# Optimization experiments

Measured on AMD Instinct MI355X. Metric: run time of the kernel, lower is better.

Reference implementation:

```python
import jax, jax.numpy as jnp
import numpy as np

B, S, E, H = 8, 1024, 1024, 16
D = E // H  # head_dim = hidden_size // num_heads


def setup_inputs() -> dict:
    key = jax.random.key(0)
    ks = jax.random.split(key, 9)
    s = 0.02
    return {
        "h":  jax.random.normal(ks[0], (B, S, E), jnp.float32),
        # per-head projection weights stacked over heads; torch Linear(E, D) -> stored [E, D] (x @ W)
        "Wq": jax.random.normal(ks[1], (H, E, D), jnp.float32) * s,
        "bq": jax.random.normal(ks[2], (H, D), jnp.float32) * s,
        "Wk": jax.random.normal(ks[3], (H, E, D), jnp.float32) * s,
        "bk": jax.random.normal(ks[4], (H, D), jnp.float32) * s,
        "Wv": jax.random.normal(ks[5], (H, E, D), jnp.float32) * s,  # dead weight: original passes h as value
        "bv": jax.random.normal(ks[6], (H, D), jnp.float32) * s,
        "Wo": jax.random.normal(ks[7], (E, E), jnp.float32) * s,
        "bo": jax.random.normal(ks[8], (E,), jnp.float32) * s,
    }


def reference(h, Wq, bq, Wk, bk, Wv, bv, Wo, bo):
    # Batched over all heads at once instead of the original Python loop.
    q = jnp.einsum('bse,hed->bhsd', h, Wq) + bq[None, :, None, :]   # [B,H,S,D]
    k = jnp.einsum('bse,hed->bhsd', h, Wk) + bk[None, :, None, :]   # [B,H,S,D]
    # v is computed in the original module but NOT used (do_attention gets h as value)
    _v = jnp.einsum('bse,hed->bhsd', h, Wv) + bv[None, :, None, :]
    scale = 1.0 / jnp.sqrt(jnp.asarray(D, h.dtype))
    scores = jnp.einsum('bhsd,bhtd->bhst', q, k) * scale            # [B,H,S,T]
    # original: F.softmax(scores, dim=1) on per-head [B,S,T] -> query axis = axis 2 here
    weights = jax.nn.softmax(scores, axis=2)
    ctx = jnp.einsum('bhst,bte->bhse', weights, h)                  # value = h (embed_dim), per original
    # torch.cat over dim=1 of per-head [B,S,E] outputs -> [B, H*S, E]
    x = ctx.reshape(B, H * S, E)
    return x @ Wo + bo
```

## Files before the change

kernel.cpp:

```cpp
#include <hip/hip_runtime.h>

#define B_ 8
#define S_ 1024
#define E_ 1024
#define H_ 16
#define D_ 64

typedef __attribute__((ext_vector_type(8))) __bf16 bf16x8;
typedef __attribute__((ext_vector_type(4))) float f32x4;
typedef __attribute__((ext_vector_type(4))) unsigned short u16x4;
typedef __attribute__((ext_vector_type(8))) unsigned short u16x8;

static __device__ __forceinline__ unsigned short f2bf(float f) {
  union { float f; unsigned int u; } v; v.f = f;
  unsigned int r = v.u + 0x7FFFu + ((v.u >> 16) & 1u);
  return (unsigned short)(r >> 16);
}

#define MFMA16(a, b, c) __builtin_amdgcn_mfma_f32_16x16x32_bf16((a), (b), (c), 0, 0, 0)

__global__ void cast_f32_bf16_kernel(const float* __restrict__ src,
                                     unsigned short* __restrict__ dst, int n4) {
  int i = blockIdx.x * 256 + threadIdx.x;
  if (i >= n4) return;
  float4 v = reinterpret_cast<const float4*>(src)[i];
  u16x4 o;
  o[0] = f2bf(v.x); o[1] = f2bf(v.y); o[2] = f2bf(v.z); o[3] = f2bf(v.w);
  reinterpret_cast<u16x4*>(dst)[i] = o;
}

__global__ void transpose_cast_kernel(const float* __restrict__ src,
                                      unsigned short* __restrict__ dst,
                                      int rows, int cols) {
  __shared__ unsigned short tile[64][65];
  const float* s = src + (size_t)blockIdx.z * rows * cols;
  unsigned short* d = dst + (size_t)blockIdx.z * rows * cols;
  int rb = blockIdx.y * 64, cb = blockIdx.x * 64;
#pragma unroll
  for (int k = 0; k < 16; k++) {
    int idx = threadIdx.x + 256 * k;
    int r = idx >> 6, c = idx & 63;
    tile[r][c] = f2bf(s[(size_t)(rb + r) * cols + cb + c]);
  }
  __syncthreads();
#pragma unroll
  for (int k = 0; k < 16; k++) {
    int idx = threadIdx.x + 256 * k;
    int r = idx >> 6, c = idx & 63;
    d[(size_t)(cb + r) * rows + rb + c] = tile[c][r];
  }
}

__launch_bounds__(256)
__global__ void gemm_G_kernel(const unsigned short* __restrict__ hb,
                              const unsigned short* __restrict__ WoT,
                              unsigned short* __restrict__ Gt) {
  int mblk = blockIdx.x, nblk = blockIdx.y, b = blockIdx.z;
  const unsigned short* A = hb + (size_t)b * S_ * E_;
  int tid = threadIdx.x, l = tid & 63, w = tid >> 6;
  int ws = w & 1, wc = w >> 1, lr = l & 15, lg = l >> 4;
  f32x4 acc[4][4] = {};
  int ar[4], bc[4];
#pragma unroll
  for (int i = 0; i < 4; i++) ar[i] = mblk * 128 + ws * 64 + i * 16 + lr;
#pragma unroll
  for (int j = 0; j < 4; j++) bc[j] = nblk * 128 + wc * 64 + j * 16 + lr;
  for (int k0 = 0; k0 < E_; k0 += 32) {
    bf16x8 a[4], bb[4];
#pragma unroll
    for (int i = 0; i < 4; i++)
      a[i] = *reinterpret_cast<const bf16x8*>(A + (size_t)ar[i] * E_ + k0 + lg * 8);
#pragma unroll
    for (int j = 0; j < 4; j++)
      bb[j] = *reinterpret_cast<const bf16x8*>(WoT + (size_t)bc[j] * E_ + k0 + lg * 8);
#pragma unroll
    for (int i = 0; i < 4; i++)
#pragma unroll
      for (int j = 0; j < 4; j++)
        acc[i][j] = MFMA16(a[i], bb[j], acc[i][j]);
  }
#pragma unroll
  for (int i = 0; i < 4; i++) {
    int t0 = mblk * 128 + ws * 64 + i * 16 + lg * 4;
#pragma unroll
    for (int j = 0; j < 4; j++) {
      u16x4 p;
#pragma unroll
      for (int r = 0; r < 4; r++) p[r] = f2bf(acc[i][j][r]);
      int e = bc[j];
      size_t addr = (((size_t)b * 4 + (e >> 8)) * 32 + (t0 >> 5)) * 8192 +
                    (size_t)(e & 255) * 32 + (t0 & 31);
      *reinterpret_cast<u16x4*>(Gt + addr) = p;
    }
  }
}

__launch_bounds__(256)
__global__ void proj_qk_kernel(const unsigned short* __restrict__ hb,
                               const unsigned short* __restrict__ WqT,
                               const unsigned short* __restrict__ WkT,
                               const float* __restrict__ bq,
                               const float* __restrict__ bk,
                               unsigned short* __restrict__ Qb,
                               unsigned short* __restrict__ Kb) {
  int sblk = blockIdx.x, z = blockIdx.y;
  int b = z >> 4, h = z & 15;
  const unsigned short* A = hb + (size_t)b * S_ * E_;
  const unsigned short* Btq = WqT + (size_t)h * D_ * E_;
  const unsigned short* Btk = WkT + (size_t)h * D_ * E_;
  int tid = threadIdx.x, l = tid & 63, w = tid >> 6;
  int ws = w & 1, wc = w >> 1, lr = l & 15, lg = l >> 4;
  f32x4 accq[4][2] = {}, acck[4][2] = {};
  int ar[4], bc[2];
#pragma unroll
  for (int i = 0; i < 4; i++) ar[i] = sblk * 128 + ws * 64 + i * 16 + lr;
#pragma unroll
  for (int j = 0; j < 2; j++) bc[j] = wc * 32 + j * 16 + lr;
  for (int k0 = 0; k0 < E_; k0 += 32) {
    bf16x8 a[4], bbq[2], bbk[2];
#pragma unroll
    for (int i = 0; i < 4; i++)
      a[i] = *reinterpret_cast<const bf16x8*>(A + (size_t)ar[i] * E_ + k0 + lg * 8);
#pragma unroll
    for (int j = 0; j < 2; j++) {
      bbq[j] = *reinterpret_cast<const bf16x8*>(Btq + (size_t)bc[j] * E_ + k0 + lg * 8);
      bbk[j] = *reinterpret_cast<const bf16x8*>(Btk + (size_t)bc[j] * E_ + k0 + lg * 8);
    }
#pragma unroll
    for (int i = 0; i < 4; i++)
#pragma unroll
      for (int j = 0; j < 2; j++) {
        accq[i][j] = MFMA16(a[i], bbq[j], accq[i][j]);
        acck[i][j] = MFMA16(a[i], bbk[j], acck[i][j]);
      }
  }
  unsigned short* oq = Qb + (size_t)z * S_ * D_;
  unsigned short* ok = Kb + (size_t)z * S_ * D_;
#pragma unroll
  for (int j = 0; j < 2; j++) {
    float bvq = bq[h * D_ + bc[j]], bvk = bk[h * D_ + bc[j]];
#pragma unroll
    for (int i = 0; i < 4; i++)
#pragma unroll
      for (int r = 0; r < 4; r++) {
        int s = sblk * 128 + ws * 64 + i * 16 + lg * 4 + r;
        oq[(size_t)s * D_ + bc[j]] = f2bf(accq[i][j][r] + bvq);
        ok[(size_t)s * D_ + bc[j]] = f2bf(acck[i][j][r] + bvk);
      }
  }
}

__launch_bounds__(256)
__global__ void stats_kernel(const unsigned short* __restrict__ Qb,
                             const unsigned short* __restrict__ Kb,
                             float* __restrict__ c) {
  int tblk = blockIdx.x, z = blockIdx.y;
  const unsigned short* Q = Qb + (size_t)z * S_ * D_;
  const unsigned short* K = Kb + (size_t)z * S_ * D_;
  int tid = threadIdx.x, l = tid & 63, w = tid >> 6;
  int lr = l & 15, lg = l >> 4;
  int tb = tblk * 256 + w * 64;
  const float scale = 0.125f;
  bf16x8 kb[4][2];
#pragma unroll
  for (int j = 0; j < 4; j++)
#pragma unroll
    for (int ks = 0; ks < 2; ks++)
      kb[j][ks] = *reinterpret_cast<const bf16x8*>(
          K + (size_t)(tb + j * 16 + lr) * D_ + ks * 32 + lg * 8);
  float m[4], zz[4];
#pragma unroll
  for (int j = 0; j < 4; j++) { m[j] = -1e30f; zz[j] = 0.f; }
  for (int s0 = 0; s0 < S_; s0 += 32) {
    bf16x8 aq[2][2];
#pragma unroll
    for (int sf = 0; sf < 2; sf++)
#pragma unroll
      for (int ks = 0; ks < 2; ks++)
        aq[sf][ks] = *reinterpret_cast<const bf16x8*>(
            Q + (size_t)(s0 + sf * 16 + lr) * D_ + ks * 32 + lg * 8);
    f32x4 acc[2][4] = {};
#pragma unroll
    for (int sf = 0; sf < 2; sf++)
#pragma unroll
      for (int j = 0; j < 4; j++) {
        acc[sf][j] = MFMA16(aq[sf][0], kb[j][0], acc[sf][j]);
        acc[sf][j] = MFMA16(aq[sf][1], kb[j][1], acc[sf][j]);
      }
#pragma unroll
    for (int j = 0; j < 4; j++) {
      float v[8];
#pragma unroll
      for (int sf = 0; sf < 2; sf++)
#pragma unroll
        for (int r = 0; r < 4; r++) v[sf * 4 + r] = acc[sf][j][r] * scale;
      float mx = m[j];
#pragma unroll
      for (int t = 0; t < 8; t++) mx = fmaxf(mx, v[t]);
      float sum = 0.f;
#pragma unroll
      for (int t = 0; t < 8; t++) sum += __expf(v[t] - mx);
      zz[j] = zz[j] * __expf(m[j] - mx) + sum;
      m[j] = mx;
    }
  }
#pragma unroll
  for (int j = 0; j < 4; j++) {
    float mj = m[j], zj = zz[j];
#pragma unroll
    for (int off = 16; off <= 32; off <<= 1) {
      float om = __shfl_xor(mj, off, 64);
      float oz = __shfl_xor(zj, off, 64);
      float mn = fmaxf(mj, om);
      zj = zj * __expf(mj - mn) + oz * __expf(om - mn);
      mj = mn;
    }
    if (l < 16) c[(size_t)z * S_ + tb + j * 16 + lr] = mj + __logf(zj);
  }
}

__launch_bounds__(256, 2)
__global__ void attn_kernel(const unsigned short* __restrict__ Qb,
                            const unsigned short* __restrict__ Kb,
                            const unsigned short* __restrict__ Gt,
                            const float* __restrict__ cst,
                            const float* __restrict__ bo,
                            float* __restrict__ out) {
  int sblk = blockIdx.x, eblk = blockIdx.y, z = blockIdx.z;
  int b = z >> 4, h = z & 15;
  __shared__ unsigned short Ks[2][32][72];
  __shared__ unsigned short Gs[256][40];
  __shared__ unsigned short Ps[128][40];
  int tid = threadIdx.x, l = tid & 63, w = tid >> 6;
  int lr = l & 15, lg = l >> 4;
  int ws = w & 1, we = w >> 1;
  const unsigned short* Q = Qb + (size_t)z * S_ * D_ + (size_t)sblk * 128 * D_;
  const unsigned short* K = Kb + (size_t)z * S_ * D_;
  const unsigned short* Gb = Gt + (((size_t)b * 4 + eblk) * 32) * 8192;
  const float* cz = cst + (size_t)z * S_;
  const float scale = 0.125f;

  bf16x8 q[2][2];
#pragma unroll
  for (int sf = 0; sf < 2; sf++)
#pragma unroll
    for (int ks = 0; ks < 2; ks++)
      q[sf][ks] = *reinterpret_cast<const bf16x8*>(
          Q + (size_t)(w * 32 + sf * 16 + lr) * D_ + ks * 32 + lg * 8);

  int krow = tid >> 3, kc8 = (tid & 7) * 8;
  u16x8 kreg, greg[4];

  kreg = *reinterpret_cast<const u16x8*>(K + (size_t)krow * D_ + kc8);
#pragma unroll
  for (int i = 0; i < 4; i++)
    greg[i] = *reinterpret_cast<const u16x8*>(Gb + (tid + 256 * i) * 8);
  *reinterpret_cast<u16x8*>(&Ks[0][krow][kc8]) = kreg;
#pragma unroll
  for (int i = 0; i < 4; i++) {
    int cid = tid + 256 * i;
    *reinterpret_cast<u16x8*>(&Gs[cid >> 2][(cid & 3) * 8]) = greg[i];
  }
  kreg = *reinterpret_cast<const u16x8*>(K + (size_t)(32 + krow) * D_ + kc8);
#pragma unroll
  for (int i = 0; i < 4; i++)
    greg[i] = *reinterpret_cast<const u16x8*>(Gb + 8192 + (tid + 256 * i) * 8);
  __syncthreads();

  f32x4 acc[4][8] = {};

  for (int it = 0; it < 32; ++it) {
    int cur = it & 1, nxt = cur ^ 1;
    int t0 = it * 32;
    *reinterpret_cast<u16x8*>(&Ks[nxt][krow][kc8]) = kreg;
    {
      int tk = t0 + 64; if (tk >= S_) tk = 0;
      kreg = *reinterpret_cast<const u16x8*>(K + (size_t)(tk + krow) * D_ + kc8);
    }
    {
      bf16x8 ka[2][2];
#pragma unroll
      for (int tf = 0; tf < 2; tf++)
#pragma unroll
        for (int ks = 0; ks < 2; ks++)
          ka[tf][ks] = *reinterpret_cast<const bf16x8*>(&Ks[cur][tf * 16 + lr][ks * 32 + lg * 8]);
      f32x4 sa[2][2] = {};
#pragma unroll
      for (int tf = 0; tf < 2; tf++)
#pragma unroll
        for (int sf = 0; sf < 2; sf++) {
          sa[tf][sf] = MFMA16(ka[tf][0], q[sf][0], sa[tf][sf]);
          sa[tf][sf] = MFMA16(ka[tf][1], q[sf][1], sa[tf][sf]);
        }
#pragma unroll
      for (int tf = 0; tf < 2; tf++) {
        f32x4 cv = *reinterpret_cast<const f32x4*>(cz + t0 + tf * 16 + lg * 4);
#pragma unroll
        for (int sf = 0; sf < 2; sf++) {
          u16x4 p;
#pragma unroll
          for (int r = 0; r < 4; r++)
            p[r] = f2bf(__expf(sa[tf][sf][r] * scale - cv[r]));
          *reinterpret_cast<u16x4*>(&Ps[w * 32 + sf * 16 + lr][tf * 16 + lg * 4]) = p;
        }
      }
    }
    __syncthreads();
    {
      bf16x8 ap[4], bg[8];
#pragma unroll
      for (int i = 0; i < 4; i++)
        ap[i] = *reinterpret_cast<const bf16x8*>(&Ps[ws * 64 + i * 16 + lr][lg * 8]);
#pragma unroll
      for (int j = 0; j < 8; j++)
        bg[j] = *reinterpret_cast<const bf16x8*>(&Gs[we * 128 + j * 16 + lr][lg * 8]);
      __builtin_amdgcn_s_setprio(1);
#pragma unroll
      for (int i = 0; i < 4; i++)
#pragma unroll
        for (int j = 0; j < 8; j++)
          acc[i][j] = MFMA16(ap[i], bg[j], acc[i][j]);
      __builtin_amdgcn_s_setprio(0);
    }
    __syncthreads();
    {
#pragma unroll
      for (int i = 0; i < 4; i++) {
        int cid = tid + 256 * i;
        *reinterpret_cast<u16x8*>(&Gs[cid >> 2][(cid & 3) * 8]) = greg[i];
      }
      int tg = (it + 2) & 31;
#pragma unroll
      for (int i = 0; i < 4; i++)
        greg[i] = *reinterpret_cast<const u16x8*>(Gb + (size_t)tg * 8192 + (tid + 256 * i) * 8);
    }
  }

  float bov[8];
#pragma unroll
  for (int j = 0; j < 8; j++) bov[j] = bo[eblk * 256 + we * 128 + j * 16 + lr];
#pragma unroll
  for (int i = 0; i < 4; i++)
#pragma unroll
    for (int j = 0; j < 8; j++)
#pragma unroll
      for (int r = 0; r < 4; r++) {
        int srow = sblk * 128 + ws * 64 + i * 16 + lg * 4 + r;
        size_t R = (size_t)h * S_ + srow;
        int col = eblk * 256 + we * 128 + j * 16 + lr;
        out[((size_t)b * (H_ * S_) + R) * E_ + col] = acc[i][j][r] + bov[j];
      }
}

extern "C" void kernel_launch(void* const* d_in, const int* in_sizes, int n_in,
                              void* d_out, int out_size, void* d_ws, size_t ws_size,
                              hipStream_t stream) {
  const float* h  = (const float*)d_in[0];
  const float* Wq = (const float*)d_in[1];
  const float* bq = (const float*)d_in[2];
  const float* Wk = (const float*)d_in[3];
  const float* bk = (const float*)d_in[4];
  const float* Wo = (const float*)d_in[7];
  const float* bo = (const float*)d_in[8];
  float* out = (float*)d_out;

  char* p = (char*)d_ws;
  unsigned short* hb  = (unsigned short*)p; p += (size_t)B_ * S_ * E_ * 2;
  unsigned short* WoT = (unsigned short*)p; p += (size_t)E_ * E_ * 2;
  unsigned short* WqT = (unsigned short*)p; p += (size_t)H_ * D_ * E_ * 2;
  unsigned short* WkT = (unsigned short*)p; p += (size_t)H_ * D_ * E_ * 2;
  unsigned short* Qb  = (unsigned short*)p; p += (size_t)B_ * H_ * S_ * D_ * 2;
  unsigned short* Kb  = (unsigned short*)p; p += (size_t)B_ * H_ * S_ * D_ * 2;
  unsigned short* Gt  = (unsigned short*)p; p += (size_t)B_ * E_ * S_ * 2;
  float*          cst = (float*)p;          p += (size_t)B_ * H_ * S_ * 4;

  int n4 = B_ * S_ * E_ / 4;
  cast_f32_bf16_kernel<<<dim3(n4 / 256), 256, 0, stream>>>(h, hb, n4);
  transpose_cast_kernel<<<dim3(16, 16, 1), 256, 0, stream>>>(Wo, WoT, E_, E_);
  transpose_cast_kernel<<<dim3(1, 16, H_), 256, 0, stream>>>(Wq, WqT, E_, D_);
  transpose_cast_kernel<<<dim3(1, 16, H_), 256, 0, stream>>>(Wk, WkT, E_, D_);
  gemm_G_kernel<<<dim3(8, 8, B_), 256, 0, stream>>>(hb, WoT, Gt);
  proj_qk_kernel<<<dim3(8, B_ * H_), 256, 0, stream>>>(hb, WqT, WkT, bq, bk, Qb, Kb);
  stats_kernel<<<dim3(S_ / 256, B_ * H_), 256, 0, stream>>>(Qb, Kb, cst);
  attn_kernel<<<dim3(8, 4, B_ * H_), 256, 0, stream>>>(Qb, Kb, Gt, cst, bo, out);
}
```

Measured before the change: 691.2 us.

## Software-pipeline attention loop with double-buffered P/G and direct K loads

Restructures the attention kernel main loop so the P·G MFMA for window it-1 runs alongside the QK^T score and exp computation for window it. P and G are double-buffered in shared memory, which cuts the barriers per iteration from two to one, and the K tile is read straight from global memory into registers instead of being staged through LDS. It also swaps the software bf16 rounding for a hardware conversion and uses exp2 with a pre-scaled log-sum-exp constant. The cost is more LDS use, which may lower occupancy, plus possibly higher global-load latency for K.

Measured after the change: 745.7 us. +7.9%, slower.

```diff
diff --git a/kernel.cpp b/kernel.cpp
--- a/kernel.cpp
+++ b/kernel.cpp
@@ -11,11 +11,18 @@
 typedef __attribute__((ext_vector_type(4))) unsigned short u16x4;
 typedef __attribute__((ext_vector_type(8))) unsigned short u16x8;
 
-static __device__ __forceinline__ unsigned short f2bf(float f) {
-  union { float f; unsigned int u; } v; v.f = f;
-  unsigned int r = v.u + 0x7FFFu + ((v.u >> 16) & 1u);
-  return (unsigned short)(r >> 16);
-}
+static __device__ __forceinline__ unsigned short f2bf_hw(float f) {
+  union { __bf16 b; unsigned short u; } v;
+  v.b = (__bf16)f;
+  return v.u;
+}
+
+#if __has_builtin(__builtin_amdgcn_exp2f)
+#define EXP2(x) __builtin_amdgcn_exp2f(x)
+#else
+#define EXP2(x) exp2f(x)
+#endif
+#define SCALE2 0.18033688f
 
 #define MFMA16(a, b, c) __builtin_amdgcn_mfma_f32_16x16x32_bf16((a), (b), (c), 0, 0, 0)
 
@@ -25,7 +32,7 @@
   if (i >= n4) return;
   float4 v = reinterpret_cast<const float4*>(src)[i];
   u16x4 o;
-  o[0] = f2bf(v.x); o[1] = f2bf(v.y); o[2] = f2bf(v.z); o[3] = f2bf(v.w);
+  o[0] = f2bf_hw(v.x); o[1] = f2bf_hw(v.y); o[2] = f2bf_hw(v.z); o[3] = f2bf_hw(v.w);
   reinterpret_cast<u16x4*>(dst)[i] = o;
 }
 
@@ -40,7 +47,7 @@
   for (int k = 0; k < 16; k++) {
     int idx = threadIdx.x + 256 * k;
     int r = idx >> 6, c = idx & 63;
-    tile[r][c] = f2bf(s[(size_t)(rb + r) * cols + cb + c]);
+    tile[r][c] = f2bf_hw(s[(size_t)(rb + r) * cols + cb + c]);
   }
   __syncthreads();
 #pragma unroll
@@ -86,7 +93,7 @@
     for (int j = 0; j < 4; j++) {
       u16x4 p;
 #pragma unroll
-      for (int r = 0; r < 4; r++) p[r] = f2bf(acc[i][j][r]);
+      for (int r = 0; r < 4; r++) p[r] = f2bf_hw(acc[i][j][r]);
       int e = bc[j];
       size_t addr = (((size_t)b * 4 + (e >> 8)) * 32 + (t0 >> 5)) * 8192 +
                     (size_t)(e & 255) * 32 + (t0 & 31);
@@ -144,8 +151,8 @@
 #pragma unroll
       for (int r = 0; r < 4; r++) {
         int s = sblk * 128 + ws * 64 + i * 16 + lg * 4 + r;
-        oq[(size_t)s * D_ + bc[j]] = f2bf(accq[i][j][r] + bvq);
-        ok[(size_t)s * D_ + bc[j]] = f2bf(acck[i][j][r] + bvk);
+        oq[(size_t)s * D_ + bc[j]] = f2bf_hw(accq[i][j][r] + bvq);
+        ok[(size_t)s * D_ + bc[j]] = f2bf_hw(acck[i][j][r] + bvk);
       }
   }
 }
@@ -215,7 +222,8 @@
       zj = zj * __expf(mj - mn) + oz * __expf(om - mn);
       mj = mn;
     }
-    if (l < 16) c[(size_t)z * S_ + tb + j * 16 + lr] = mj + __logf(zj);
+    if (l < 16)
+      c[(size_t)z * S_ + tb + j * 16 + lr] = (mj + __logf(zj)) * 1.44269504f;
   }
 }
 
@@ -228,9 +236,8 @@
                             float* __restrict__ out) {
   int sblk = blockIdx.x, eblk = blockIdx.y, z = blockIdx.z;
   int b = z >> 4, h = z & 15;
-  __shared__ unsigned short Ks[2][32][72];
-  __shared__ unsigned short Gs[256][40];
-  __shared__ unsigned short Ps[128][40];
+  __shared__ unsigned short Gs[2][256][40];
+  __shared__ unsigned short Ps[2][128][40];
   int tid = threadIdx.x, l = tid & 63, w = tid >> 6;
   int lr = l & 15, lg = l >> 4;
   int ws = w & 1, we = w >> 1;
@@ -238,7 +245,6 @@
   const unsigned short* K = Kb + (size_t)z * S_ * D_;
   const unsigned short* Gb = Gt + (((size_t)b * 4 + eblk) * 32) * 8192;
   const float* cz = cst + (size_t)z * S_;
-  const float scale = 0.125f;
 
   bf16x8 q[2][2];
 #pragma unroll
@@ -248,92 +254,100 @@
       q[sf][ks] = *reinterpret_cast<const bf16x8*>(
           Q + (size_t)(w * 32 + sf * 16 + lr) * D_ + ks * 32 + lg * 8);
 
-  int krow = tid >> 3, kc8 = (tid & 7) * 8;
-  u16x8 kreg, greg[4];
-
-  kreg = *reinterpret_cast<const u16x8*>(K + (size_t)krow * D_ + kc8);
+  u16x8 greg[4];
 #pragma unroll
   for (int i = 0; i < 4; i++)
-    greg[i] = *reinterpret_cast<const u16x8*>(Gb + (tid + 256 * i) * 8);
-  *reinterpret_cast<u16x8*>(&Ks[0][krow][kc8]) = kreg;
-#pragma unroll
-  for (int i = 0; i < 4; i++) {
-    int cid = tid + 256 * i;
-    *reinterpret_cast<u16x8*>(&Gs[cid >> 2][(cid & 3) * 8]) = greg[i];
-  }
-  kreg = *reinterpret_cast<const u16x8*>(K + (size_t)(32 + krow) * D_ + kc8);
-#pragma unroll
-  for (int i = 0; i < 4; i++)
-    greg[i] = *reinterpret_cast<const u16x8*>(Gb + 8192 + (tid + 256 * i) * 8);
-  __syncthreads();
+    greg[i] = *reinterpret_cast<const u16x8*>(Gb + (size_t)(tid + 256 * i) * 8);
 
   f32x4 acc[4][8] = {};
 
-  for (int it = 0; it < 32; ++it) {
-    int cur = it & 1, nxt = cur ^ 1;
-    int t0 = it * 32;
-    *reinterpret_cast<u16x8*>(&Ks[nxt][krow][kc8]) = kreg;
-    {
-      int tk = t0 + 64; if (tk >= S_) tk = 0;
-      kreg = *reinterpret_cast<const u16x8*>(K + (size_t)(tk + krow) * D_ + kc8);
-    }
-    {
-      bf16x8 ka[2][2];
-#pragma unroll
-      for (int tf = 0; tf < 2; tf++)
-#pragma unroll
-        for (int ks = 0; ks < 2; ks++)
-          ka[tf][ks] = *reinterpret_cast<const bf16x8*>(&Ks[cur][tf * 16 + lr][ks * 32 + lg * 8]);
-      f32x4 sa[2][2] = {};
-#pragma unroll
-      for (int tf = 0; tf < 2; tf++)
-#pragma unroll
-        for (int sf = 0; sf < 2; sf++) {
-          sa[tf][sf] = MFMA16(ka[tf][0], q[sf][0], sa[tf][sf]);
-          sa[tf][sf] = MFMA16(ka[tf][1], q[sf][1], sa[tf][sf]);
-        }
-#pragma unroll
-      for (int tf = 0; tf < 2; tf++) {
-        f32x4 cv = *reinterpret_cast<const f32x4*>(cz + t0 + tf * 16 + lg * 4);
-#pragma unroll
-        for (int sf = 0; sf < 2; sf++) {
-          u16x4 p;
-#pragma unroll
-          for (int r = 0; r < 4; r++)
-            p[r] = f2bf(__expf(sa[tf][sf][r] * scale - cv[r]));
-          *reinterpret_cast<u16x4*>(&Ps[w * 32 + sf * 16 + lr][tf * 16 + lg * 4]) = p;
-        }
-      }
-    }
-    __syncthreads();
-    {
-      bf16x8 ap[4], bg[8];
-#pragma unroll
-      for (int i = 0; i < 4; i++)
-        ap[i] = *reinterpret_cast<const bf16x8*>(&Ps[ws * 64 + i * 16 + lr][lg * 8]);
-#pragma unroll
-      for (int j = 0; j < 8; j++)
-        bg[j] = *reinterpret_cast<const bf16x8*>(&Gs[we * 128 + j * 16 + lr][lg * 8]);
-      __builtin_amdgcn_s_setprio(1);
-#pragma unroll
-      for (int i = 0; i < 4; i++)
-#pragma unroll
-        for (int j = 0; j < 8; j++)
-          acc[i][j] = MFMA16(ap[i], bg[j], acc[i][j]);
-      __builtin_amdgcn_s_setprio(0);
-    }
-    __syncthreads();
-    {
-#pragma unroll
-      for (int i = 0; i < 4; i++) {
-        int cid = tid + 256 * i;
-        *reinterpret_cast<u16x8*>(&Gs[cid >> 2][(cid & 3) * 8]) = greg[i];
-      }
-      int tg = (it + 2) & 31;
-#pragma unroll
-      for (int i = 0; i < 4; i++)
-        greg[i] = *reinterpret_cast<const u16x8*>(Gb + (size_t)tg * 8192 + (tid + 256 * i) * 8);
-    }
+#define WINDOW(IT, CUR)                                                           \
+  do {                                                                            \
+    int t0_ = (IT) * 32;                                                          \
+    bf16x8 ka_[2][2];                                                             \
+    _Pragma("unroll") for (int tf = 0; tf < 2; tf++)                              \
+      _Pragma("unroll") for (int ks = 0; ks < 2; ks++)                            \
+        ka_[tf][ks] = *reinterpret_cast<const bf16x8*>(                           \
+            K + (size_t)(t0_ + tf * 16 + lr) * D_ + ks * 32 + lg * 8);            \
+    _Pragma("unroll") for (int i = 0; i < 4; i++) {                               \
+      int cid = tid + 256 * i;                                                    \
+      *reinterpret_cast<u16x8*>(&Gs[CUR][cid >> 2][(cid & 3) * 8]) = greg[i];     \
+    }                                                                             \
+    {                                                                             \
+      int tg_ = ((IT) + 1) & 31;                                                  \
+      _Pragma("unroll") for (int i = 0; i < 4; i++)                               \
+        greg[i] = *reinterpret_cast<const u16x8*>(                                \
+            Gb + (size_t)tg_ * 8192 + (size_t)(tid + 256 * i) * 8);               \
+    }                                                                             \
+    if ((IT) > 0) {                                                 \
+      bf16x8 ap_[4], bg_[4];                                                      \
+      _Pragma("unroll") for (int i = 0; i < 4; i++)                               \
+        ap_[i] = *reinterpret_cast<const bf16x8*>(                                \
+            &Ps[(CUR) ^ 1][ws * 64 + i * 16 + lr][lg * 8]);                       \
+      __builtin_amdgcn_s_setprio(1);                                              \
+      _Pragma("unroll") for (int j = 0; j < 4; j++)                               \
+        bg_[j] = *reinterpret_cast<const bf16x8*>(                                \
+            &Gs[(CUR) ^ 1][we * 128 + j * 16 + lr][lg * 8]);                      \
+      _Pragma("unroll") for (int i = 0; i < 4; i++)                               \
+        _Pragma("unroll") for (int j = 0; j < 4; j++)                             \
+          acc[i][j] = MFMA16(ap_[i], bg_[j], acc[i][j]);                          \
+      _Pragma("unroll") for (int j = 0; j < 4; j++)                               \
+        bg_[j] = *reinterpret_cast<const bf16x8*>(                                \
+            &Gs[(CUR) ^ 1][we * 128 + (j + 4) * 16 + lr][lg * 8]);                \
+      _Pragma("unroll") for (int i = 0; i < 4; i++)                               \
+        _Pragma("unroll") for (int j = 0; j < 4; j++)                             \
+          acc[i][j + 4] = MFMA16(ap_[i], bg_[j], acc[i][j + 4]);                  \
+      __builtin_amdgcn_s_setprio(0);                                              \
+    }                                                                             \
+    {                                              \
+      f32x4 sa_[2][2] = {};                                                       \
+      _Pragma("unroll") for (int tf = 0; tf < 2; tf++)                            \
+        _Pragma("unroll") for (int sf = 0; sf < 2; sf++) {                        \
+          sa_[tf][sf] = MFMA16(ka_[tf][0], q[sf][0], sa_[tf][sf]);                \
+          sa_[tf][sf] = MFMA16(ka_[tf][1], q[sf][1], sa_[tf][sf]);                \
+        }                                                                         \
+      _Pragma("unroll") for (int tf = 0; tf < 2; tf++) {                          \
+        f32x4 cv_ = *reinterpret_cast<const f32x4*>(cz + t0_ + tf * 16 + lg * 4); \
+        _Pragma("unroll") for (int sf = 0; sf < 2; sf++) {                        \
+          u16x4 p_;                                                               \
+          _Pragma("unroll") for (int r = 0; r < 4; r++)                           \
+            p_[r] = f2bf_hw(EXP2(fmaf(sa_[tf][sf][r], SCALE2, -cv_[r])));         \
+          *reinterpret_cast<u16x4*>(                                              \
+              &Ps[CUR][w * 32 + sf * 16 + lr][tf * 16 + lg * 4]) = p_;            \
+        }                                                                         \
+      }                                                                           \
+    }                                                                             \
+    __syncthreads();                                                              \
+  } while (0)
+
+  for (int it2 = 0; it2 < 16; ++it2) {
+    int it = it2 * 2;
+    WINDOW(it, 0);
+    WINDOW(it + 1, 1);
+  }
+#undef WINDOW
+
+  {
+    bf16x8 ap_[4], bg_[4];
+#pragma unroll
+    for (int i = 0; i < 4; i++)
+      ap_[i] = *reinterpret_cast<const bf16x8*>(&Ps[1][ws * 64 + i * 16 + lr][lg * 8]);
+#pragma unroll
+    for (int j = 0; j < 4; j++)
+      bg_[j] = *reinterpret_cast<const bf16x8*>(&Gs[1][we * 128 + j * 16 + lr][lg * 8]);
+#pragma unroll
+    for (int i = 0; i < 4; i++)
+#pragma unroll
+      for (int j = 0; j < 4; j++)
+        acc[i][j] = MFMA16(ap_[i], bg_[j], acc[i][j]);
+#pragma unroll
+    for (int j = 0; j < 4; j++)
+      bg_[j] = *reinterpret_cast<const bf16x8*>(&Gs[1][we * 128 + (j + 4) * 16 + lr][lg * 8]);
+#pragma unroll
+    for (int i = 0; i < 4; i++)
+#pragma unroll
+      for (int j = 0; j < 4; j++)
+        acc[i][j + 4] = MFMA16(ap_[i], bg_[j], acc[i][j + 4]);
   }
 
   float bov[8];
```

## Restructure attention kernel to per-wave tiles reading K and G directly

Applied to the files above, without the earlier changes.

Attention now gives each wave its own 32-row query slice with a private P tile and reads K and G fragments straight from global memory, with no shared-memory staging and no block barriers. The output tile narrows to 128 columns, so the grid doubles along E, the G layout is re-blocked to match, and the launch bound rises to 3 blocks per CU. Softmax switches to exp2 with pre-scaled log-sum-exp constants, and a hardware bf16 conversion replaces the manual rounding. This removes syncs and LDS traffic but reloads K and G from global or cache per wave and doubles the number of QK score recomputations.

New measurement: 1.268 ms. +83.4%, slower.

```diff
diff --git a/kernel.cpp b/kernel.cpp
--- a/kernel.cpp
+++ b/kernel.cpp
@@ -11,11 +11,18 @@
 typedef __attribute__((ext_vector_type(4))) unsigned short u16x4;
 typedef __attribute__((ext_vector_type(8))) unsigned short u16x8;
 
-static __device__ __forceinline__ unsigned short f2bf(float f) {
-  union { float f; unsigned int u; } v; v.f = f;
-  unsigned int r = v.u + 0x7FFFu + ((v.u >> 16) & 1u);
-  return (unsigned short)(r >> 16);
-}
+static __device__ __forceinline__ unsigned short f2bf_hw(float f) {
+  union { __bf16 b; unsigned short u; } v;
+  v.b = (__bf16)f;
+  return v.u;
+}
+
+#if __has_builtin(__builtin_amdgcn_exp2f)
+#define EXP2(x) __builtin_amdgcn_exp2f(x)
+#else
+#define EXP2(x) exp2f(x)
+#endif
+#define SCALE2 0.18033688f
 
 #define MFMA16(a, b, c) __builtin_amdgcn_mfma_f32_16x16x32_bf16((a), (b), (c), 0, 0, 0)
 
@@ -25,7 +32,7 @@
   if (i >= n4) return;
   float4 v = reinterpret_cast<const float4*>(src)[i];
   u16x4 o;
-  o[0] = f2bf(v.x); o[1] = f2bf(v.y); o[2] = f2bf(v.z); o[3] = f2bf(v.w);
+  o[0] = f2bf_hw(v.x); o[1] = f2bf_hw(v.y); o[2] = f2bf_hw(v.z); o[3] = f2bf_hw(v.w);
   reinterpret_cast<u16x4*>(dst)[i] = o;
 }
 
@@ -40,7 +47,7 @@
   for (int k = 0; k < 16; k++) {
     int idx = threadIdx.x + 256 * k;
     int r = idx >> 6, c = idx & 63;
-    tile[r][c] = f2bf(s[(size_t)(rb + r) * cols + cb + c]);
+    tile[r][c] = f2bf_hw(s[(size_t)(rb + r) * cols + cb + c]);
   }
   __syncthreads();
 #pragma unroll
@@ -86,10 +93,10 @@
     for (int j = 0; j < 4; j++) {
       u16x4 p;
 #pragma unroll
-      for (int r = 0; r < 4; r++) p[r] = f2bf(acc[i][j][r]);
+      for (int r = 0; r < 4; r++) p[r] = f2bf_hw(acc[i][j][r]);
       int e = bc[j];
-      size_t addr = (((size_t)b * 4 + (e >> 8)) * 32 + (t0 >> 5)) * 8192 +
-                    (size_t)(e & 255) * 32 + (t0 & 31);
+      size_t addr = (((size_t)b * 8 + (e >> 7)) * 32 + (t0 >> 5)) * 4096 +
+                    (size_t)(e & 127) * 32 + (t0 & 31);
       *reinterpret_cast<u16x4*>(Gt + addr) = p;
     }
   }
@@ -144,8 +151,8 @@
 #pragma unroll
       for (int r = 0; r < 4; r++) {
         int s = sblk * 128 + ws * 64 + i * 16 + lg * 4 + r;
-        oq[(size_t)s * D_ + bc[j]] = f2bf(accq[i][j][r] + bvq);
-        ok[(size_t)s * D_ + bc[j]] = f2bf(acck[i][j][r] + bvk);
+        oq[(size_t)s * D_ + bc[j]] = f2bf_hw(accq[i][j][r] + bvq);
+        ok[(size_t)s * D_ + bc[j]] = f2bf_hw(acck[i][j][r] + bvk);
       }
   }
 }
@@ -215,11 +222,12 @@
       zj = zj * __expf(mj - mn) + oz * __expf(om - mn);
       mj = mn;
     }
-    if (l < 16) c[(size_t)z * S_ + tb + j * 16 + lr] = mj + __logf(zj);
-  }
-}
-
-__launch_bounds__(256, 2)
+    if (l < 16)
+      c[(size_t)z * S_ + tb + j * 16 + lr] = (mj + __logf(zj)) * 1.44269504f;
+  }
+}
+
+__launch_bounds__(256, 3)
 __global__ void attn_kernel(const unsigned short* __restrict__ Qb,
                             const unsigned short* __restrict__ Kb,
                             const unsigned short* __restrict__ Gt,
@@ -228,17 +236,13 @@
                             float* __restrict__ out) {
   int sblk = blockIdx.x, eblk = blockIdx.y, z = blockIdx.z;
   int b = z >> 4, h = z & 15;
-  __shared__ unsigned short Ks[2][32][72];
-  __shared__ unsigned short Gs[256][40];
-  __shared__ unsigned short Ps[128][40];
+  __shared__ unsigned short Ps[4][32][40];
   int tid = threadIdx.x, l = tid & 63, w = tid >> 6;
   int lr = l & 15, lg = l >> 4;
-  int ws = w & 1, we = w >> 1;
-  const unsigned short* Q = Qb + (size_t)z * S_ * D_ + (size_t)sblk * 128 * D_;
+  const unsigned short* Q = Qb + (size_t)z * S_ * D_ + (size_t)(sblk * 128 + w * 32) * D_;
   const unsigned short* K = Kb + (size_t)z * S_ * D_;
-  const unsigned short* Gb = Gt + (((size_t)b * 4 + eblk) * 32) * 8192;
+  const unsigned short* Gb = Gt + (((size_t)b * 8 + eblk) * 32) * 4096;
   const float* cz = cst + (size_t)z * S_;
-  const float scale = 0.125f;
 
   bf16x8 q[2][2];
 #pragma unroll
@@ -246,109 +250,78 @@
 #pragma unroll
     for (int ks = 0; ks < 2; ks++)
       q[sf][ks] = *reinterpret_cast<const bf16x8*>(
-          Q + (size_t)(w * 32 + sf * 16 + lr) * D_ + ks * 32 + lg * 8);
-
-  int krow = tid >> 3, kc8 = (tid & 7) * 8;
-  u16x8 kreg, greg[4];
-
-  kreg = *reinterpret_cast<const u16x8*>(K + (size_t)krow * D_ + kc8);
-#pragma unroll
-  for (int i = 0; i < 4; i++)
-    greg[i] = *reinterpret_cast<const u16x8*>(Gb + (tid + 256 * i) * 8);
-  *reinterpret_cast<u16x8*>(&Ks[0][krow][kc8]) = kreg;
-#pragma unroll
-  for (int i = 0; i < 4; i++) {
-    int cid = tid + 256 * i;
-    *reinterpret_cast<u16x8*>(&Gs[cid >> 2][(cid & 3) * 8]) = greg[i];
-  }
-  kreg = *reinterpret_cast<const u16x8*>(K + (size_t)(32 + krow) * D_ + kc8);
-#pragma unroll
-  for (int i = 0; i < 4; i++)
-    greg[i] = *reinterpret_cast<const u16x8*>(Gb + 8192 + (tid + 256 * i) * 8);
-  __syncthreads();
-
-  f32x4 acc[4][8] = {};
-
-  for (int it = 0; it < 32; ++it) {
-    int cur = it & 1, nxt = cur ^ 1;
-    int t0 = it * 32;
-    *reinterpret_cast<u16x8*>(&Ks[nxt][krow][kc8]) = kreg;
-    {
-      int tk = t0 + 64; if (tk >= S_) tk = 0;
-      kreg = *reinterpret_cast<const u16x8*>(K + (size_t)(tk + krow) * D_ + kc8);
-    }
-    {
-      bf16x8 ka[2][2];
-#pragma unroll
-      for (int tf = 0; tf < 2; tf++)
-#pragma unroll
-        for (int ks = 0; ks < 2; ks++)
-          ka[tf][ks] = *reinterpret_cast<const bf16x8*>(&Ks[cur][tf * 16 + lr][ks * 32 + lg * 8]);
-      f32x4 sa[2][2] = {};
-#pragma unroll
-      for (int tf = 0; tf < 2; tf++)
-#pragma unroll
-        for (int sf = 0; sf < 2; sf++) {
-          sa[tf][sf] = MFMA16(ka[tf][0], q[sf][0], sa[tf][sf]);
-          sa[tf][sf] = MFMA16(ka[tf][1], q[sf][1], sa[tf][sf]);
-        }
-#pragma unroll
-      for (int tf = 0; tf < 2; tf++) {
-        f32x4 cv = *reinterpret_cast<const f32x4*>(cz + t0 + tf * 16 + lg * 4);
-#pragma unroll
-        for (int sf = 0; sf < 2; sf++) {
-          u16x4 p;
-#pragma unroll
-          for (int r = 0; r < 4; r++)
-            p[r] = f2bf(__expf(sa[tf][sf][r] * scale - cv[r]));
-          *reinterpret_cast<u16x4*>(&Ps[w * 32 + sf * 16 + lr][tf * 16 + lg * 4]) = p;
-        }
-      }
-    }
-    __syncthreads();
-    {
-      bf16x8 ap[4], bg[8];
-#pragma unroll
-      for (int i = 0; i < 4; i++)
-        ap[i] = *reinterpret_cast<const bf16x8*>(&Ps[ws * 64 + i * 16 + lr][lg * 8]);
-#pragma unroll
-      for (int j = 0; j < 8; j++)
-        bg[j] = *reinterpret_cast<const bf16x8*>(&Gs[we * 128 + j * 16 + lr][lg * 8]);
-      __builtin_amdgcn_s_setprio(1);
-#pragma unroll
-      for (int i = 0; i < 4; i++)
-#pragma unroll
-        for (int j = 0; j < 8; j++)
-          acc[i][j] = MFMA16(ap[i], bg[j], acc[i][j]);
-      __builtin_amdgcn_s_setprio(0);
-    }
-    __syncthreads();
-    {
-#pragma unroll
-      for (int i = 0; i < 4; i++) {
-        int cid = tid + 256 * i;
-        *reinterpret_cast<u16x8*>(&Gs[cid >> 2][(cid & 3) * 8]) = greg[i];
-      }
-      int tg = (it + 2) & 31;
-#pragma unroll
-      for (int i = 0; i < 4; i++)
-        greg[i] = *reinterpret_cast<const u16x8*>(Gb + (size_t)tg * 8192 + (tid + 256 * i) * 8);
-    }
+          Q + (size_t)(sf * 16 + lr) * D_ + ks * 32 + lg * 8);
+
+  f32x4 acc[2][8] = {};
+
+#pragma unroll 2
+  for (int t0 = 0; t0 < S_; t0 += 32) {
+    bf16x8 ka[2][2];
+#pragma unroll
+    for (int tf = 0; tf < 2; tf++)
+#pragma unroll
+      for (int ks = 0; ks < 2; ks++)
+        ka[tf][ks] = *reinterpret_cast<const bf16x8*>(
+            K + (size_t)(t0 + tf * 16 + lr) * D_ + ks * 32 + lg * 8);
+
+    f32x4 sa[2][2] = {};
+#pragma unroll
+    for (int tf = 0; tf < 2; tf++)
+#pragma unroll
+      for (int sf = 0; sf < 2; sf++) {
+        sa[tf][sf] = MFMA16(ka[tf][0], q[sf][0], sa[tf][sf]);
+        sa[tf][sf] = MFMA16(ka[tf][1], q[sf][1], sa[tf][sf]);
+      }
+
+#pragma unroll
+    for (int tf = 0; tf < 2; tf++) {
+      f32x4 cv = *reinterpret_cast<const f32x4*>(cz + t0 + tf * 16 + lg * 4);
+#pragma unroll
+      for (int sf = 0; sf < 2; sf++) {
+        u16x4 p;
+#pragma unroll
+        for (int r = 0; r < 4; r++)
+          p[r] = f2bf_hw(EXP2(fmaf(sa[tf][sf][r], SCALE2, -cv[r])));
+        *reinterpret_cast<u16x4*>(&Ps[w][sf * 16 + lr][tf * 16 + lg * 4]) = p;
+      }
+    }
+
+    bf16x8 ap[2];
+#pragma unroll
+    for (int sf = 0; sf < 2; sf++)
+      ap[sf] = *reinterpret_cast<const bf16x8*>(&Ps[w][sf * 16 + lr][lg * 8]);
+
+    const unsigned short* Gw = Gb + (size_t)(t0 >> 5) * 4096;
+    __builtin_amdgcn_s_setprio(1);
+#pragma unroll
+    for (int jh = 0; jh < 2; jh++) {
+      bf16x8 bg[4];
+#pragma unroll
+      for (int j = 0; j < 4; j++)
+        bg[j] = *reinterpret_cast<const bf16x8*>(
+            Gw + (size_t)((jh * 4 + j) * 16 + lr) * 32 + lg * 8);
+#pragma unroll
+      for (int sf = 0; sf < 2; sf++)
+#pragma unroll
+        for (int j = 0; j < 4; j++)
+          acc[sf][jh * 4 + j] = MFMA16(ap[sf], bg[j], acc[sf][jh * 4 + j]);
+    }
+    __builtin_amdgcn_s_setprio(0);
   }
 
   float bov[8];
 #pragma unroll
-  for (int j = 0; j < 8; j++) bov[j] = bo[eblk * 256 + we * 128 + j * 16 + lr];
-#pragma unroll
-  for (int i = 0; i < 4; i++)
+  for (int j = 0; j < 8; j++) bov[j] = bo[eblk * 128 + j * 16 + lr];
+#pragma unroll
+  for (int sf = 0; sf < 2; sf++)
 #pragma unroll
     for (int j = 0; j < 8; j++)
 #pragma unroll
       for (int r = 0; r < 4; r++) {
-        int srow = sblk * 128 + ws * 64 + i * 16 + lg * 4 + r;
-        size_t R = (size_t)h * S_ + srow;
-        int col = eblk * 256 + we * 128 + j * 16 + lr;
-        out[((size_t)b * (H_ * S_) + R) * E_ + col] = acc[i][j][r] + bov[j];
+        int s = sblk * 128 + w * 32 + sf * 16 + lg * 4 + r;
+        int col = eblk * 128 + j * 16 + lr;
+        out[((size_t)b * (H_ * S_) + (size_t)h * S_ + s) * E_ + col] =
+            acc[sf][j][r] + bov[j];
       }
 }
 
@@ -382,5 +355,5 @@
   gemm_G_kernel<<<dim3(8, 8, B_), 256, 0, stream>>>(hb, WoT, Gt);
   proj_qk_kernel<<<dim3(8, B_ * H_), 256, 0, stream>>>(hb, WqT, WkT, bq, bk, Qb, Kb);
   stats_kernel<<<dim3(S_ / 256, B_ * H_), 256, 0, stream>>>(Qb, Kb, cst);
-  attn_kernel<<<dim3(8, 4, B_ * H_), 256, 0, stream>>>(Qb, Kb, Gt, cst, bo, out);
-}
+  attn_kernel<<<dim3(8, 8, B_ * H_), 256, 0, stream>>>(Qb, Kb, Gt, cst, bo, out);
+}
```
